# Optimization experiments

Measured on AMD Instinct MI355X. Metric: run time of the kernel, lower is better.

The kernel has to match this reference:

```python
import jax, jax.numpy as jnp
import numpy as np

TRIANGLE_TABLE = np.array([
    [-1, -1, -1, -1, -1, -1], [1, 0, 2, -1, -1, -1], [4, 0, 3, -1, -1, -1], [1, 4, 2, 1, 3, 4],
    [3, 1, 5, -1, -1, -1], [2, 3, 0, 2, 5, 3], [1, 4, 0, 1, 5, 4], [4, 2, 5, -1, -1, -1],
    [4, 5, 2, -1, -1, -1], [4, 1, 0, 4, 5, 1], [3, 2, 0, 3, 5, 2], [1, 3, 5, -1, -1, -1],
    [4, 1, 2, 4, 3, 1], [3, 0, 4, -1, -1, -1], [2, 0, 1, -1, -1, -1], [-1, -1, -1, -1, -1, -1]], np.int32)
NUM_TRIANGLES_TABLE = np.array([0, 1, 1, 2, 1, 2, 2, 1, 1, 2, 2, 1, 2, 1, 1, 0], np.int32)
BASE_TET_EDGES = np.array([0, 1, 0, 2, 0, 3, 1, 2, 1, 3, 2, 3], np.int32)


def _make_tet_grid(R):
    # Regular grid in [0,1]^3, each cube split into 6 tets along the 0-7 diagonal.
    r1 = R + 1
    gi, gj, gk = np.meshgrid(np.arange(r1), np.arange(r1), np.arange(r1), indexing='ij')
    verts = (np.stack([gi, gj, gk], -1).reshape(-1, 3) / R).astype(np.float32)  # (Nv,3)
    ci, cj, ck = np.meshgrid(np.arange(R), np.arange(R), np.arange(R), indexing='ij')
    ci, cj, ck = ci.ravel(), cj.ravel(), ck.ravel()
    def vid(dx, dy, dz):
        return ((ci + dx) * r1 + (cj + dy)) * r1 + (ck + dz)
    corners = [vid((c >> 2) & 1, (c >> 1) & 1, c & 1) for c in range(8)]
    tet_corners = [(0, 1, 3, 7), (0, 3, 2, 7), (0, 2, 6, 7), (0, 6, 4, 7), (0, 4, 5, 7), (0, 5, 1, 7)]
    tets = np.stack([np.stack([corners[a] for a in t], -1) for t in tet_corners], 1).reshape(-1, 4)
    return verts, tets.astype(np.int32)


def setup_inputs() -> dict:
    R = 64
    verts, tets = _make_tet_grid(R)
    key = jax.random.key(0)
    k1, k2 = jax.random.split(key)
    level = jax.random.normal(k1, (verts.shape[0],), dtype=jnp.float32)
    deformation = jax.random.normal(k2, (verts.shape[0], 3), dtype=jnp.float32)
    return {
        'level': level,
        'deformation': deformation,
        'grid_vertices': jnp.asarray(verts),
        'tet_indices': jnp.asarray(tets),
        'resolution': R,
    }


def reference(level, deformation, grid_vertices, tet_indices, resolution):
    # normalize_grid_deformation: (range_hi - range_lo)/res * tanh(offsets), range = (0,1)
    pos = grid_vertices + jnp.tanh(deformation) / resolution  # (Nv,3)
    occ = level > 0                                           # (Nv,)
    occ_f = occ[tet_indices]                                  # (F,4)
    occ_sum = occ_f.sum(-1)
    valid = (occ_sum > 0) & (occ_sum < 4)
    vt = tet_indices[valid]                                   # (Fv,4)
    occ_valid = occ_f[valid]                                  # (Fv,4)
    # per-tet edges, each sorted (min,max) -> dedup
    edges = vt[:, jnp.asarray(BASE_TET_EDGES)].reshape(-1, 2)  # (6*Fv,2)
    edges = jnp.sort(edges, axis=1)
    unique_edges, idx_map = jnp.unique(edges, axis=0, return_inverse=True)
    idx_map = idx_map.reshape(-1)
    # edges that actually cross the isosurface (exactly one endpoint inside)
    mask_edges = occ[unique_edges].sum(-1) == 1               # (U,)
    mapping = jnp.where(mask_edges, jnp.cumsum(mask_edges.astype(jnp.int32)) - 1, -1)
    idx_map = mapping[idx_map].reshape(-1, 6)                 # (Fv,6)
    interp_v = unique_edges[mask_edges]                       # (M,2)
    # linear interpolation of crossing point along each edge
    ep = pos[interp_v]                                        # (M,2,3)
    es = level[interp_v] * jnp.array([1.0, -1.0], dtype=level.dtype)  # (M,2) = [sdf0, -sdf1]
    w = es[:, ::-1] / es.sum(1, keepdims=True)                # (M,2) = [-sdf1, sdf0]/(sdf0-sdf1)
    verts_out = (ep * w[:, :, None]).sum(1)                   # (M,3)
    # triangle table lookup
    v_id = jnp.array([1, 2, 4, 8], dtype=jnp.int32)
    tetindex = (occ_valid.astype(jnp.int32) * v_id).sum(-1)   # (Fv,)
    tri_tab = jnp.asarray(TRIANGLE_TABLE)
    num_tri = jnp.asarray(NUM_TRIANGLES_TABLE)[tetindex]
    m1 = num_tri == 1
    m2 = num_tri == 2
    f1 = jnp.take_along_axis(idx_map[m1], tri_tab[tetindex[m1]][:, :3], axis=1).reshape(-1, 3)
    f2 = jnp.take_along_axis(idx_map[m2], tri_tab[tetindex[m2]][:, :6], axis=1).reshape(-1, 3)
    faces = jnp.concatenate([f1, f2], axis=0)                 # (Nf,3)
    return verts_out, faces
```

## Files before the change

kernel.cpp:

```cpp
#include <hip/hip_runtime.h>
#include <math.h>


typedef unsigned long long ull;

#define ST_LD(p)    __hip_atomic_load((p), __ATOMIC_RELAXED, __HIP_MEMORY_SCOPE_AGENT)
#define ST_ST(p,v)  __hip_atomic_store((p), (v), __ATOMIC_RELAXED, __HIP_MEMORY_SCOPE_AGENT)

__device__ __forceinline__ float fast_tanh(float x) {
    float e = __expf(2.0f * x);
    return __fdividef(e - 1.0f, e + 1.0f);
}

__device__ __constant__ int c_tri_tab[16][6] = {
    {-1,-1,-1,-1,-1,-1},{1,0,2,-1,-1,-1},{4,0,3,-1,-1,-1},{1,4,2,1,3,4},
    {3,1,5,-1,-1,-1},{2,3,0,2,5,3},{1,4,0,1,5,4},{4,2,5,-1,-1,-1},
    {4,5,2,-1,-1,-1},{4,1,0,4,5,1},{3,2,0,3,5,2},{1,3,5,-1,-1,-1},
    {4,1,2,4,3,1},{3,0,4,-1,-1,-1},{2,0,1,-1,-1,-1},{-1,-1,-1,-1,-1,-1}};
__device__ __constant__ int c_num_tri[16] = {0,1,1,2,1,2,2,1,1,2,2,1,2,1,1,0};
__device__ __constant__ int c_tc[6][4] = {{0,1,3,7},{0,3,2,7},{0,2,6,7},{0,6,4,7},{0,4,5,7},{0,5,1,7}};
__device__ __constant__ int c_te[6][6] = {
    {(0<<3)|0,(0<<3)|2,(0<<3)|6,(1<<3)|1,(1<<3)|5,(3<<3)|3},
    {(0<<3)|2,(0<<3)|1,(0<<3)|6,(2<<3)|0,(3<<3)|3,(2<<3)|4},
    {(0<<3)|1,(0<<3)|5,(0<<3)|6,(2<<3)|3,(2<<3)|4,(6<<3)|0},
    {(0<<3)|5,(0<<3)|3,(0<<3)|6,(4<<3)|1,(6<<3)|0,(4<<3)|2},
    {(0<<3)|3,(0<<3)|4,(0<<3)|6,(4<<3)|0,(4<<3)|2,(5<<3)|1},
    {(0<<3)|4,(0<<3)|0,(0<<3)|6,(1<<3)|3,(5<<3)|1,(1<<3)|5}};

#define TAG      (1ull << 62)
#define PMASK    ((1ull << 60) - 1ull)
#define READY(s) (((s) >> 62) == 1ull)

__global__ void k_vert(const float* __restrict__ level, const float* __restrict__ deform,
                       int NV, int r1, float invR,
                       ull* __restrict__ stateA, ull* __restrict__ prefS,
                       unsigned* __restrict__ rankWord, ull* __restrict__ cubeInfo,
                       int* __restrict__ totals, ull* __restrict__ dtab,
                       float* __restrict__ out) {
    int b = blockIdx.x;
    int v = b * 256 + threadIdx.x;
    int R = r1 - 1, rsq = r1 * r1;
    bool valid = v < NV;
    float la = valid ? level[v] : 0.f;
    bool occv = valid && (la > 0.f);

    int x = 0, y = 0, z = 0, flags = 0, n1 = 0, n2 = 0, cidx = 0, ob = 0;
    bool interior = false;
    float lb[7];
    if (valid) {
        x = v / rsq; int rem = v - x * rsq; y = rem / r1; z = rem - y * r1;
        bool bx = x < R, by = y < R, bz = z < R;
        interior = bx && by && bz;
        bool inb[7] = {bz, by, by && bz, bx, bx && bz, bx && by, interior};
        int deltas[7] = {1, r1, r1 + 1, rsq, rsq + 1, rsq + r1, rsq + r1 + 1};
        ob = occv ? 1 : 0;
        for (int j = 0; j < 7; j++) {
            float l = inb[j] ? level[v + deltas[j]] : 0.f;
            lb[j] = l;
            bool o = inb[j] && (l > 0.f);
            ob |= (o ? 1 : 0) << (j + 1);
            if (inb[j] && (o != occv)) flags |= 1 << j;
        }
        if (interior) {
            cidx = ((x * R) + y) * R + z;
            for (int k = 0; k < 6; k++) {
                int ti = ((ob >> c_tc[k][0]) & 1) | (((ob >> c_tc[k][1]) & 1) << 1)
                       | (((ob >> c_tc[k][2]) & 1) << 2) | (((ob >> c_tc[k][3]) & 1) << 3);
                int n = c_num_tri[ti];
                n1 += (n == 1); n2 += (n == 2);
            }
        }
    }
    int cnt = __popc(flags);
    int pk = n1 | (n2 << 16);
    int lane = threadIdx.x & 63, wv = threadIdx.x >> 6;
    int inclE = cnt, inclT = pk;
    for (int o = 1; o < 64; o <<= 1) {
        int tE = __shfl_up(inclE, o);
        int tT = __shfl_up(inclT, o);
        if (lane >= o) { inclE += tE; inclT += tT; }
    }
    __shared__ int wE[4], wT[4];
    __shared__ ull sExcl;
    if (lane == 63) { wE[wv] = inclE; wT[wv] = inclT; }
    __syncthreads();

    if (wv == 0) {
        int eb = 0, t1b = 0, t2b = 0;
        if (lane == 0) {
            eb = wE[0] + wE[1] + wE[2] + wE[3];
            int tb = wT[0] + wT[1] + wT[2] + wT[3];
            t1b = tb & 0xffff; t2b = tb >> 16;
            ST_ST(&stateA[b], TAG | ((ull)eb << 40) | ((ull)t1b << 20) | (ull)t2b);
        }
        ull sum = 0;
        for (int w = 0; 64 * w < b; w++) {
            int i = b - 1 - 64 * w - lane;
            ull pv = (i >= 0) ? ST_LD(&prefS[i]) : 0;
            ull pm = __ballot(i >= 0 && READY(pv));
            int Lp = pm ? (__ffsll((long long)pm) - 1) : 64;
            ull val = 0;
            if (i >= 0 && lane < Lp) {
                ull s;
                do { s = ST_LD(&stateA[i]); } while (!READY(s));
                val = s & PMASK;
            } else if (i >= 0 && lane == Lp) {
                val = pv & PMASK;
            }
            for (int o = 1; o < 64; o <<= 1) val += __shfl_xor(val, o);
            sum += val;
            if (Lp < 64) break;
        }
        if (lane == 0) {
            sExcl = sum;
            ull inc = sum + (((ull)eb << 40) | ((ull)t1b << 20) | (ull)t2b);
            ST_ST(&prefS[b], TAG | inc);
            if (b == (int)gridDim.x - 1) {
                totals[0] = (int)((inc >> 40) & 0xFFFFF);
                totals[1] = (int)((inc >> 20) & 0xFFFFF);
                totals[2] = (int)(inc & 0xFFFFF);
            }
        }
    }
    __syncthreads();

    ull ex = sExcl;
    int exclE = (int)((ex >> 40) & 0xFFFFF);
    int excl1 = (int)((ex >> 20) & 0xFFFFF);
    int excl2 = (int)(ex & 0xFFFFF);
    int woffE = 0, woffT = 0;
    for (int w2 = 0; w2 < wv; w2++) { woffE += wE[w2]; woffT += wT[w2]; }
    int rank0 = exclE + woffE + inclE - cnt;
    int tExcl = woffT + inclT - pk;
    if (interior)
        cubeInfo[cidx] = (ull)(unsigned)ob
                       | ((ull)(unsigned)(excl1 + (tExcl & 0xffff)) << 8)
                       | ((ull)(unsigned)(excl2 + (tExcl >> 16)) << 28);
    if (valid)
        rankWord[v] = (unsigned)rank0 | ((unsigned)flags << 21);

    __shared__ float ldsV[5376];
    if (flags) {
        int deltas[7] = {1, r1, r1 + 1, rsq, rsq + 1, rsq + r1, rsq + r1 + 1};
        const int dxs[7] = {0, 0, 0, 1, 1, 1, 1};
        const int dys[7] = {0, 1, 1, 0, 0, 1, 1};
        const int dzs[7] = {1, 0, 1, 0, 1, 0, 1};
        float pax = x * invR + fast_tanh(deform[3 * v])     * invR;
        float pay = y * invR + fast_tanh(deform[3 * v + 1]) * invR;
        float paz = z * invR + fast_tanh(deform[3 * v + 2]) * invR;
        int r = rank0 - exclE;
        for (int j = 0; j < 7; j++) {
            if (!((flags >> j) & 1)) continue;
            int bb = v + deltas[j];
            float lbv = lb[j];
            float inv = __fdividef(1.0f, la - lbv);
            float w0 = -lbv * inv;
            float w1f = la * inv;
            float pbx = (x + dxs[j]) * invR + fast_tanh(deform[3 * bb])     * invR;
            float pby = (y + dys[j]) * invR + fast_tanh(deform[3 * bb + 1]) * invR;
            float pbz = (z + dzs[j]) * invR + fast_tanh(deform[3 * bb + 2]) * invR;
            ldsV[3 * r]     = pax * w0 + pbx * w1f;
            ldsV[3 * r + 1] = pay * w0 + pby * w1f;
            ldsV[3 * r + 2] = paz * w0 + pbz * w1f;
            r++;
        }
    }
    __syncthreads();
    int eb2 = wE[0] + wE[1] + wE[2] + wE[3];
    int tot = 3 * eb2;
    float* dstV = out + 3 * (size_t)exclE;
    for (int i = threadIdx.x; i < tot; i += 256) dstV[i] = ldsV[i];

    if (b < 8) {
        int idx = b * 256 + threadIdx.x;
        int obt = idx >> 3, k = idx & 7;
        ull w = 0;
        if (k < 6) {
            int ti = ((obt >> c_tc[k][0]) & 1) | (((obt >> c_tc[k][1]) & 1) << 1)
                   | (((obt >> c_tc[k][2]) & 1) << 2) | (((obt >> c_tc[k][3]) & 1) << 3);
            int nt = c_num_tri[ti];
            int pre1 = 0, pre2 = 0;
            for (int kk = 0; kk < k; kk++) {
                int tik = ((obt >> c_tc[kk][0]) & 1) | (((obt >> c_tc[kk][1]) & 1) << 1)
                        | (((obt >> c_tc[kk][2]) & 1) << 2) | (((obt >> c_tc[kk][3]) & 1) << 3);
                int m = c_num_tri[tik];
                pre1 += (m == 1); pre2 += (m == 2);
            }
            w = (ull)nt | ((ull)pre1 << 2) | ((ull)pre2 << 5);
            for (int e = 0; e < 6; e++) {
                int le = c_tri_tab[ti][e];
                int ce = (le >= 0) ? c_te[k][le] : 0;
                w |= (ull)ce << (8 + 6 * e);
            }
        }
        dtab[idx] = w;
    }
}

__global__ void k_face(int r1, int NT,
                       const ull* __restrict__ cubeInfo,
                       const unsigned* __restrict__ rankWord,
                       const int* __restrict__ totals,
                       const ull* __restrict__ dtab,
                       float* __restrict__ out) {
    int tid = threadIdx.x;
    int t = blockIdx.x * 256 + tid;
    bool act = t < NT;
    int rsq = r1 * r1, R = r1 - 1, rr = R * R;
    ull info = 0, w = 0;
    int k = 0, v = 0, nt = 0;
    if (act) {
        int c = t / 6; k = t - c * 6;
        info = cubeInfo[c];
        w = dtab[(((int)info & 255) << 3) | k];
        nt = (int)w & 3;
        int cx = c / rr; int rem = c - cx * rr; int cy = rem / R; int cz = rem - cy * R;
        v = (cx * r1 + cy) * r1 + cz;
    }
    unsigned slot1 = act ? (unsigned)((info >> 8) & 0xFFFFF) + (unsigned)((w >> 2) & 7) : 0u;
    unsigned slot2 = act ? (unsigned)((info >> 28) & 0xFFFFF) + (unsigned)((w >> 5) & 7) : 0u;

    __shared__ unsigned sB1, sB2, sE1, sE2;
    __shared__ float lds1[768];
    __shared__ float lds2[1536];
    int lastT = NT - 1 - blockIdx.x * 256; if (lastT > 255) lastT = 255;
    if (tid == 0)     { sB1 = slot1; sB2 = slot2; }
    if (tid == lastT) { sE1 = slot1 + (nt == 1); sE2 = slot2 + (nt == 2); }
    __syncthreads();

    #define ERANK(ce_)                                                          \
        ({ int ce = (ce_);                                                      \
           int a = v + ((ce >> 5) & 1) * rsq + ((ce >> 4) & 1) * r1 + ((ce >> 3) & 1); \
           unsigned rw = rankWord[a];                                           \
           (float)((int)(rw & 0x1FFFFF) + __popc((rw >> 21) & ((1u << (ce & 7)) - 1u))); })

    if (act && nt) {
        ull we = w >> 8;
        if (nt == 1) {
            float* d = &lds1[(slot1 - sB1) * 3];
            d[0] = ERANK((int)(we) & 63);
            d[1] = ERANK((int)(we >> 6) & 63);
            d[2] = ERANK((int)(we >> 12) & 63);
        } else {
            float* d = &lds2[(slot2 - sB2) * 6];
            #pragma unroll
            for (int e = 0; e < 6; e++) d[e] = ERANK((int)(we >> (6 * e)) & 63);
        }
    }
    #undef ERANK
    __syncthreads();

    int M = totals[0], N1 = totals[1];
    float* faces = out + 3 * (size_t)M;
    int n1b = (int)(sE1 - sB1), n2b = (int)(sE2 - sB2);
    float* d1 = faces + 3 * (size_t)sB1;
    for (int i = tid; i < 3 * n1b; i += 256) d1[i] = lds1[i];
    float* d2 = faces + 3 * (size_t)N1 + 6 * (size_t)sB2;
    for (int i = tid; i < 6 * n2b; i += 256) d2[i] = lds2[i];
}

extern "C" void kernel_launch(void* const* d_in, const int* in_sizes, int n_in,
                              void* d_out, int out_size, void* d_ws, size_t ws_size,
                              hipStream_t stream) {
    const float* level  = (const float*)d_in[0];
    const float* deform = (const float*)d_in[1];
    int NV = in_sizes[0];
    int r1 = 1;
    while ((long long)r1 * r1 * r1 < (long long)NV) r1++;
    int R = r1 - 1;
    float invR = 1.0f / (float)R;

    int nb = (NV + 255) / 256;
    int NC = R * R * R;
    int NT = 6 * NC;
    int nbT = (NT + 255) / 256;

    char* w = (char*)d_ws;
    unsigned* rankWord = (unsigned*)w;
    w += (((size_t)NV * sizeof(unsigned)) + 255) & ~(size_t)255;
    ull* cubeInfo = (ull*)w;
    w += (((size_t)NC * 8) + 255) & ~(size_t)255;
    ull* stateA = (ull*)w;
    w += (((size_t)nb * 8) + 255) & ~(size_t)255;
    ull* prefS = (ull*)w;
    w += (((size_t)nb * 8) + 255) & ~(size_t)255;
    int* totals = (int*)w;
    w += 256;
    ull* dtab = (ull*)w;

    float* out = (float*)d_out;

    k_vert<<<nb, 256, 0, stream>>>(level, deform, NV, r1, invR, stateA, prefS,
                                   rankWord, cubeInfo, totals, dtab, out);
    k_face<<<nbT, 256, 0, stream>>>(r1, NT, cubeInfo, rankWord, totals, dtab, out);
}
```

Baseline: 117.9 us.

## Replace decoupled look-back with full predecessor sum; process one cube per thread in faces

The vertex kernel no longer publishes inclusive prefixes with look-back. Instead, all four waves of each block sum the local aggregates of every preceding block directly, spinning until each is ready. This removes the serial look-back chain, but the number of loads per block grows linearly with block index (about 1100 blocks). The face kernel now assigns one cube per thread instead of one tet per thread. It loads the six dtab words with vector loads and reads the 8 corner rankWords once, selecting among them in registers, which cuts redundant global loads. The cost is larger LDS use (9216 floats) and six times fewer threads.

```diff
diff --git a/kernel.cpp b/kernel.cpp
--- a/kernel.cpp
+++ b/kernel.cpp
@@ -33,7 +33,7 @@
 
 __global__ void k_vert(const float* __restrict__ level, const float* __restrict__ deform,
                        int NV, int r1, float invR,
-                       ull* __restrict__ stateA, ull* __restrict__ prefS,
+                       ull* __restrict__ stateA,
                        unsigned* __restrict__ rankWord, ull* __restrict__ cubeInfo,
                        int* __restrict__ totals, ull* __restrict__ dtab,
                        float* __restrict__ out) {
@@ -81,53 +81,43 @@
         if (lane >= o) { inclE += tE; inclT += tT; }
     }
     __shared__ int wE[4], wT[4];
-    __shared__ ull sExcl;
+    __shared__ ull sPart[4];
     if (lane == 63) { wE[wv] = inclE; wT[wv] = inclT; }
     __syncthreads();
 
-    if (wv == 0) {
-        int eb = 0, t1b = 0, t2b = 0;
-        if (lane == 0) {
-            eb = wE[0] + wE[1] + wE[2] + wE[3];
-            int tb = wT[0] + wT[1] + wT[2] + wT[3];
-            t1b = tb & 0xffff; t2b = tb >> 16;
-            ST_ST(&stateA[b], TAG | ((ull)eb << 40) | ((ull)t1b << 20) | (ull)t2b);
-        }
-        ull sum = 0;
-        for (int w = 0; 64 * w < b; w++) {
-            int i = b - 1 - 64 * w - lane;
-            ull pv = (i >= 0) ? ST_LD(&prefS[i]) : 0;
-            ull pm = __ballot(i >= 0 && READY(pv));
-            int Lp = pm ? (__ffsll((long long)pm) - 1) : 64;
-            ull val = 0;
-            if (i >= 0 && lane < Lp) {
-                ull s;
-                do { s = ST_LD(&stateA[i]); } while (!READY(s));
-                val = s & PMASK;
-            } else if (i >= 0 && lane == Lp) {
-                val = pv & PMASK;
-            }
-            for (int o = 1; o < 64; o <<= 1) val += __shfl_xor(val, o);
-            sum += val;
-            if (Lp < 64) break;
-        }
-        if (lane == 0) {
-            sExcl = sum;
-            ull inc = sum + (((ull)eb << 40) | ((ull)t1b << 20) | (ull)t2b);
-            ST_ST(&prefS[b], TAG | inc);
-            if (b == (int)gridDim.x - 1) {
-                totals[0] = (int)((inc >> 40) & 0xFFFFF);
-                totals[1] = (int)((inc >> 20) & 0xFFFFF);
-                totals[2] = (int)(inc & 0xFFFFF);
-            }
-        }
-    }
-    __syncthreads();
-
-    ull ex = sExcl;
+    if (threadIdx.x == 0) {
+        int eb = wE[0] + wE[1] + wE[2] + wE[3];
+        int tb = wT[0] + wT[1] + wT[2] + wT[3];
+        ST_ST(&stateA[b], TAG | ((ull)eb << 40) | ((ull)(tb & 0xffff) << 20) | (ull)(tb >> 16));
+    }
+    ull psum = 0;
+    for (int t = 0;; t++) {
+        int base = 64 * (4 * t + wv);
+        if (base >= b) break;
+        int i = b - 1 - (base + lane);
+        ull s = 0;
+        if (i >= 0) {
+            do { s = ST_LD(&stateA[i]); } while (!READY(s));
+            s &= PMASK;
+        }
+        psum += s;
+    }
+    for (int o = 1; o < 64; o <<= 1) psum += __shfl_xor(psum, o);
+    if (lane == 0) sPart[wv] = psum;
+    __syncthreads();
+
+    ull ex = sPart[0] + sPart[1] + sPart[2] + sPart[3];
     int exclE = (int)((ex >> 40) & 0xFFFFF);
     int excl1 = (int)((ex >> 20) & 0xFFFFF);
     int excl2 = (int)(ex & 0xFFFFF);
+    int eb2 = wE[0] + wE[1] + wE[2] + wE[3];
+    if (threadIdx.x == 0 && b == (int)gridDim.x - 1) {
+        int tb = wT[0] + wT[1] + wT[2] + wT[3];
+        ull inc = ex + (((ull)eb2 << 40) | ((ull)(tb & 0xffff) << 20) | (ull)(tb >> 16));
+        totals[0] = (int)((inc >> 40) & 0xFFFFF);
+        totals[1] = (int)((inc >> 20) & 0xFFFFF);
+        totals[2] = (int)(inc & 0xFFFFF);
+    }
     int woffE = 0, woffT = 0;
     for (int w2 = 0; w2 < wv; w2++) { woffE += wE[w2]; woffT += wT[w2]; }
     int rank0 = exclE + woffE + inclE - cnt;
@@ -166,7 +156,6 @@
         }
     }
     __syncthreads();
-    int eb2 = wE[0] + wE[1] + wE[2] + wE[3];
     int tot = 3 * eb2;
     float* dstV = out + 3 * (size_t)exclE;
     for (int i = threadIdx.x; i < tot; i += 256) dstV[i] = ldsV[i];
@@ -197,66 +186,107 @@
     }
 }
 
-__global__ void k_face(int r1, int NT,
+__device__ __forceinline__ unsigned sel8(int c, unsigned r0, unsigned r1_, unsigned r2,
+                                         unsigned r3, unsigned r4, unsigned r5,
+                                         unsigned r6, unsigned r7) {
+    unsigned a01 = (c & 1) ? r1_ : r0;
+    unsigned a23 = (c & 1) ? r3 : r2;
+    unsigned a45 = (c & 1) ? r5 : r4;
+    unsigned a67 = (c & 1) ? r7 : r6;
+    unsigned lo = (c & 2) ? a23 : a01;
+    unsigned hi = (c & 2) ? a67 : a45;
+    return (c & 4) ? hi : lo;
+}
+
+__global__ void k_face(int r1, int NC,
                        const ull* __restrict__ cubeInfo,
                        const unsigned* __restrict__ rankWord,
                        const int* __restrict__ totals,
                        const ull* __restrict__ dtab,
                        float* __restrict__ out) {
     int tid = threadIdx.x;
-    int t = blockIdx.x * 256 + tid;
-    bool act = t < NT;
+    int c = blockIdx.x * 256 + tid;
+    bool act = c < NC;
     int rsq = r1 * r1, R = r1 - 1, rr = R * R;
-    ull info = 0, w = 0;
-    int k = 0, v = 0, nt = 0;
+
+    ull info = 0;
+    ull w0 = 0, w1 = 0, w2 = 0, w3 = 0, w4 = 0, w5 = 0;
+    unsigned rw0=0,rw1=0,rw2=0,rw3=0,rw4=0,rw5=0,rw6=0,rw7=0;
     if (act) {
-        int c = t / 6; k = t - c * 6;
         info = cubeInfo[c];
-        w = dtab[(((int)info & 255) << 3) | k];
-        nt = (int)w & 3;
+        int ob = (int)info & 255;
+        const ull* dp = dtab + (ob << 3);
+        ulonglong2 p0 = *reinterpret_cast<const ulonglong2*>(dp);
+        ulonglong2 p1 = *reinterpret_cast<const ulonglong2*>(dp + 2);
+        ulonglong2 p2 = *reinterpret_cast<const ulonglong2*>(dp + 4);
+        w0 = p0.x; w1 = p0.y; w2 = p1.x; w3 = p1.y; w4 = p2.x; w5 = p2.y;
         int cx = c / rr; int rem = c - cx * rr; int cy = rem / R; int cz = rem - cy * R;
-        v = (cx * r1 + cy) * r1 + cz;
-    }
-    unsigned slot1 = act ? (unsigned)((info >> 8) & 0xFFFFF) + (unsigned)((w >> 2) & 7) : 0u;
-    unsigned slot2 = act ? (unsigned)((info >> 28) & 0xFFFFF) + (unsigned)((w >> 5) & 7) : 0u;
+        int v = (cx * r1 + cy) * r1 + cz;
+        rw0 = rankWord[v];             rw1 = rankWord[v + 1];
+        rw2 = rankWord[v + r1];        rw3 = rankWord[v + r1 + 1];
+        rw4 = rankWord[v + rsq];       rw5 = rankWord[v + rsq + 1];
+        rw6 = rankWord[v + rsq + r1];  rw7 = rankWord[v + rsq + r1 + 1];
+    }
+    unsigned r1c = (unsigned)((info >> 8) & 0xFFFFF);
+    unsigned r2c = (unsigned)((info >> 28) & 0xFFFFF);
+    int nt5 = (int)w5 & 3;
+    int n1c = (((int)w5 >> 2) & 7) + (nt5 == 1);
+    int n2c = (((int)w5 >> 5) & 7) + (nt5 == 2);
 
     __shared__ unsigned sB1, sB2, sE1, sE2;
-    __shared__ float lds1[768];
-    __shared__ float lds2[1536];
-    int lastT = NT - 1 - blockIdx.x * 256; if (lastT > 255) lastT = 255;
-    if (tid == 0)     { sB1 = slot1; sB2 = slot2; }
-    if (tid == lastT) { sE1 = slot1 + (nt == 1); sE2 = slot2 + (nt == 2); }
-    __syncthreads();
+    __shared__ float ldsF[9216];
+    int lastT = NC - 1 - blockIdx.x * 256; if (lastT > 255) lastT = 255;
+    if (tid == 0)     { sB1 = r1c; sB2 = r2c; }
+    if (tid == lastT) { sE1 = r1c + (unsigned)n1c; sE2 = r2c + (unsigned)n2c; }
+    __syncthreads();
+
+    int n1b = (int)(sE1 - sB1), n2b = (int)(sE2 - sB2);
+    float* Lr1 = ldsF;
+    float* Lr2 = ldsF + 3 * n1b;
 
     #define ERANK(ce_)                                                          \
         ({ int ce = (ce_);                                                      \
-           int a = v + ((ce >> 5) & 1) * rsq + ((ce >> 4) & 1) * r1 + ((ce >> 3) & 1); \
-           unsigned rw = rankWord[a];                                           \
+           unsigned rw = sel8(ce >> 3, rw0,rw1,rw2,rw3,rw4,rw5,rw6,rw7);        \
            (float)((int)(rw & 0x1FFFFF) + __popc((rw >> 21) & ((1u << (ce & 7)) - 1u))); })
 
-    if (act && nt) {
-        ull we = w >> 8;
-        if (nt == 1) {
-            float* d = &lds1[(slot1 - sB1) * 3];
-            d[0] = ERANK((int)(we) & 63);
-            d[1] = ERANK((int)(we >> 6) & 63);
-            d[2] = ERANK((int)(we >> 12) & 63);
-        } else {
-            float* d = &lds2[(slot2 - sB2) * 6];
-            #pragma unroll
-            for (int e = 0; e < 6; e++) d[e] = ERANK((int)(we >> (6 * e)) & 63);
-        }
+    if (act) {
+        int local1 = (int)(r1c - sB1);
+        int local2 = (int)(r2c - sB2);
+        #define DO_TET(wk) do {                                                 \
+            int nt = (int)(wk) & 3;                                             \
+            if (nt) {                                                           \
+                ull we = (wk) >> 8;                                             \
+                if (nt == 1) {                                                  \
+                    int s = local1 + (((int)(wk) >> 2) & 7);                    \
+                    float* d = &Lr1[3 * s];                                     \
+                    d[0] = ERANK((int)(we) & 63);                               \
+                    d[1] = ERANK((int)(we >> 6) & 63);                          \
+                    d[2] = ERANK((int)(we >> 12) & 63);                         \
+                } else {                                                        \
+                    int s = local2 + (((int)(wk) >> 5) & 7);                    \
+                    float* d = &Lr2[6 * s];                                     \
+                    d[0] = ERANK((int)(we) & 63);                               \
+                    d[1] = ERANK((int)(we >> 6) & 63);                          \
+                    d[2] = ERANK((int)(we >> 12) & 63);                         \
+                    d[3] = ERANK((int)(we >> 18) & 63);                         \
+                    d[4] = ERANK((int)(we >> 24) & 63);                         \
+                    d[5] = ERANK((int)(we >> 30) & 63);                         \
+                }                                                               \
+            }                                                                   \
+        } while (0)
+        DO_TET(w0); DO_TET(w1); DO_TET(w2); DO_TET(w3); DO_TET(w4); DO_TET(w5);
+        #undef DO_TET
     }
     #undef ERANK
     __syncthreads();
 
     int M = totals[0], N1 = totals[1];
     float* faces = out + 3 * (size_t)M;
-    int n1b = (int)(sE1 - sB1), n2b = (int)(sE2 - sB2);
     float* d1 = faces + 3 * (size_t)sB1;
-    for (int i = tid; i < 3 * n1b; i += 256) d1[i] = lds1[i];
+    for (int i = tid; i < 3 * n1b; i += 256) d1[i] = ldsF[i];
     float* d2 = faces + 3 * (size_t)N1 + 6 * (size_t)sB2;
-    for (int i = tid; i < 6 * n2b; i += 256) d2[i] = lds2[i];
+    const float* s2 = ldsF + 3 * n1b;
+    for (int i = tid; i < 6 * n2b; i += 256) d2[i] = s2[i];
 }
 
 extern "C" void kernel_launch(void* const* d_in, const int* in_sizes, int n_in,
@@ -272,8 +302,7 @@
 
     int nb = (NV + 255) / 256;
     int NC = R * R * R;
-    int NT = 6 * NC;
-    int nbT = (NT + 255) / 256;
+    int nbC = (NC + 255) / 256;
 
     char* w = (char*)d_ws;
     unsigned* rankWord = (unsigned*)w;
@@ -282,15 +311,13 @@
     w += (((size_t)NC * 8) + 255) & ~(size_t)255;
     ull* stateA = (ull*)w;
     w += (((size_t)nb * 8) + 255) & ~(size_t)255;
-    ull* prefS = (ull*)w;
-    w += (((size_t)nb * 8) + 255) & ~(size_t)255;
     int* totals = (int*)w;
     w += 256;
     ull* dtab = (ull*)w;
 
     float* out = (float*)d_out;
 
-    k_vert<<<nb, 256, 0, stream>>>(level, deform, NV, r1, invR, stateA, prefS,
+    k_vert<<<nb, 256, 0, stream>>>(level, deform, NV, r1, invR, stateA,
                                    rankWord, cubeInfo, totals, dtab, out);
-    k_face<<<nbT, 256, 0, stream>>>(r1, NT, cubeInfo, rankWord, totals, dtab, out);
-}
+    k_face<<<nbC, 256, 0, stream>>>(r1, NC, cubeInfo, rankWord, totals, dtab, out);
+}
```

New measurement: 113.5 us. 1.04x faster.
